# Kernel tuning notes

Measured on AMD Instinct MI355X. Metric: run time of the kernel, lower is better.

Reference implementation:

```python
import jax, jax.numpy as jnp
import numpy as np

DIM = 64
HEADS = 4
N_NODES = 50000
N_EDGES = 800000
NEG_SLOPE = 0.2


def setup_inputs() -> dict:
    key = jax.random.key(0)
    k1, k2, k3, k4, k5 = jax.random.split(key, 5)
    meta_x = jax.random.normal(k1, (N_NODES, DIM), dtype=jnp.float32)
    meta_edge_index = jax.random.randint(k2, (2, N_EDGES), 0, N_NODES, dtype=jnp.int64)
    # GATConv params: shared source/dest Linear (no bias), per-head attention vecs, output bias.
    glorot = float(np.sqrt(2.0 / (DIM + HEADS * DIM)))
    W = jax.random.normal(k3, (DIM, HEADS * DIM), dtype=jnp.float32) * glorot  # x @ W
    att_src = jax.random.normal(k4, (1, HEADS, DIM), dtype=jnp.float32) * glorot
    att_dst = jax.random.normal(k5, (1, HEADS, DIM), dtype=jnp.float32) * glorot
    bias = jnp.zeros((DIM,), dtype=jnp.float32)
    return {"meta_x": meta_x, "meta_edge_index": meta_edge_index,
            "W": W, "att_src": att_src, "att_dst": att_dst, "bias": bias}


def reference(meta_x, meta_edge_index, W, att_src, att_dst, bias):
    N = meta_x.shape[0]
    # PyG GATConv default: add self-loops
    loops = jnp.arange(N, dtype=meta_edge_index.dtype)
    edge = jnp.concatenate([meta_edge_index, jnp.stack([loops, loops])], axis=1)
    src, dst = edge[0], edge[1]

    x = (meta_x @ W).reshape(N, HEADS, DIM)            # [N, H, C]
    a_src = jnp.sum(x * att_src, axis=-1)              # [N, H]
    a_dst = jnp.sum(x * att_dst, axis=-1)              # [N, H]

    logits = a_src[src] + a_dst[dst]                   # [E, H]
    logits = jax.nn.leaky_relu(logits, NEG_SLOPE)

    # segment softmax over edges grouped by destination node
    seg_max = jax.ops.segment_max(logits, dst, num_segments=N)   # [N, H]
    ex = jnp.exp(logits - seg_max[dst])
    seg_sum = jax.ops.segment_sum(ex, dst, num_segments=N)
    alpha = ex / (seg_sum[dst] + 1e-16)                # [E, H]

    msg = x[src] * alpha[:, :, None]                   # [E, H, C]
    out = jax.ops.segment_sum(msg, dst, num_segments=N)  # [N, H, C]
    # concat=False -> mean over heads, then bias
    return out.mean(axis=1) + bias
```

## Files before the change

### kernel.cpp

```cpp
#include <hip/hip_runtime.h>
#include <hip/hip_bf16.h>
#include <math.h>

#define MAXDEG 64

__device__ __forceinline__ float lrelu(float v) { return v > 0.0f ? v : 0.2f * v; }

__global__ void prep_kernel(int4* __restrict__ cnt4, int n4,
                            const float* __restrict__ W, const float* __restrict__ att_src,
                            const float* __restrict__ att_dst, float* __restrict__ wsrc,
                            float* __restrict__ wdst) {
  int idx = blockIdx.x * 256 + threadIdx.x;
  for (int i = idx; i < n4; i += gridDim.x * 256) cnt4[i] = make_int4(0, 0, 0, 0);
  if (blockIdx.x == 0) {
    int t = threadIdx.x;
    int h = t >> 6, k = t & 63;
    const float* wrow = W + (size_t)k * 256 + h * 64;
    const float* as = att_src + h * 64;
    const float* ad = att_dst + h * 64;
    float ss = 0.f, sd = 0.f;
#pragma unroll
    for (int c = 0; c < 64; ++c) {
      float w = wrow[c];
      ss = fmaf(w, as[c], ss);
      sd = fmaf(w, ad[c], sd);
    }
    wsrc[k * 4 + h] = ss;
    wdst[k * 4 + h] = sd;
  }
}

__global__ void nattn_kernel(const float* __restrict__ x, const float4* __restrict__ wsrc4,
                             const float4* __restrict__ wdst4, float4* __restrict__ asrc4,
                             float4* __restrict__ adst4, __hip_bfloat16* __restrict__ xh,
                             int N) {
  int lane = threadIdx.x & 63;
  int n = blockIdx.x * 4 + (threadIdx.x >> 6);
  if (n >= N) return;
  float xv = x[(size_t)n * 64 + lane];
  xh[(size_t)n * 64 + lane] = __float2bfloat16(xv);
  float4 ws = wsrc4[lane], wd = wdst4[lane];
  float s0 = xv * ws.x, s1 = xv * ws.y, s2 = xv * ws.z, s3 = xv * ws.w;
  float d0 = xv * wd.x, d1 = xv * wd.y, d2 = xv * wd.z, d3 = xv * wd.w;
#pragma unroll
  for (int m = 1; m < 64; m <<= 1) {
    s0 += __shfl_xor(s0, m, 64); s1 += __shfl_xor(s1, m, 64);
    s2 += __shfl_xor(s2, m, 64); s3 += __shfl_xor(s3, m, 64);
    d0 += __shfl_xor(d0, m, 64); d1 += __shfl_xor(d1, m, 64);
    d2 += __shfl_xor(d2, m, 64); d3 += __shfl_xor(d3, m, 64);
  }
  if (lane == 0) {
    asrc4[n] = make_float4(s0, s1, s2, s3);
    adst4[n] = make_float4(d0, d1, d2, d3);
  }
}

__global__ void hist_kernel(const int* __restrict__ ei, int* __restrict__ counts,
                            int E, int N) {
  int e = blockIdx.x * 256 + threadIdx.x;
  int ET = E + N;
  if (e >= ET) return;
  int dst = (e < E) ? ei[(size_t)E + e] : (e - E);
  atomicAdd(&counts[dst], 1);
}

__global__ void scatter_kernel(const int* __restrict__ ei, int* __restrict__ cursor,
                               int* __restrict__ src_sorted, int E, int N) {
  int e = blockIdx.x * 256 + threadIdx.x;
  int ET = E + N;
  if (e >= ET) return;
  int src, dst;
  if (e < E) {
    src = ei[e];
    dst = ei[(size_t)E + e];
  } else {
    src = dst = e - E;
  }
  int pos = atomicAdd(&cursor[dst], 1);
  src_sorted[pos] = src;
}

__global__ void hist4_kernel(const int* __restrict__ ei, int* __restrict__ counts,
                             int E, int N) {
  int i = blockIdx.x * 256 + threadIdx.x;
  int E4 = E >> 2;
  if (i < E4) {
    int4 d = ((const int4*)(ei + E))[i];
    atomicAdd(&counts[d.x], 1);
    atomicAdd(&counts[d.y], 1);
    atomicAdd(&counts[d.z], 1);
    atomicAdd(&counts[d.w], 1);
  } else if (i < E4 + N) {
    atomicAdd(&counts[i - E4], 1);
  }
}

__global__ void scatter8_kernel(const int* __restrict__ ei, int* __restrict__ cursor,
                                int* __restrict__ srt, int E, int N) {
  int slice = blockIdx.x & 7;
  int bid = blockIdx.x >> 3;
  int nb = gridDim.x >> 3;
  int chunk = (N + 7) >> 3;
  int lo = slice * chunk;
  int hi = lo + chunk; if (hi > N) hi = N;
  int E4 = E >> 2;
  const int4* s4p = (const int4*)ei;
  const int4* d4p = (const int4*)(ei + E);
  int stride = nb * 256;
  for (int i = bid * 256 + threadIdx.x; i < E4; i += stride) {
    int4 d4 = d4p[i];
    bool bx = (d4.x >= lo && d4.x < hi), by = (d4.y >= lo && d4.y < hi);
    bool bz = (d4.z >= lo && d4.z < hi), bw = (d4.w >= lo && d4.w < hi);
    if (!(bx || by || bz || bw)) continue;
    int4 s4 = s4p[i];
    if (bx) { int p = atomicAdd(&cursor[d4.x], 1); srt[p] = s4.x; }
    if (by) { int p = atomicAdd(&cursor[d4.y], 1); srt[p] = s4.y; }
    if (bz) { int p = atomicAdd(&cursor[d4.z], 1); srt[p] = s4.z; }
    if (bw) { int p = atomicAdd(&cursor[d4.w], 1); srt[p] = s4.w; }
  }
  for (int n = lo + bid * 256 + threadIdx.x; n < hi; n += stride) {
    int p = atomicAdd(&cursor[n], 1);
    srt[p] = n;
  }
}

__global__ void scanA_kernel(const int* __restrict__ cnt, int* __restrict__ tsum, int N) {
  int b = blockIdx.x, t = threadIdx.x;
  int idx = b * 256 + t;
  int v = (idx < N) ? cnt[idx] : 0;
#pragma unroll
  for (int m = 1; m < 64; m <<= 1) v += __shfl_xor(v, m, 64);
  __shared__ int ws[4];
  if ((t & 63) == 0) ws[t >> 6] = v;
  __syncthreads();
  if (t == 0) tsum[b] = ws[0] + ws[1] + ws[2] + ws[3];
}

__global__ void scanBC_kernel(const int* __restrict__ cnt, const int* __restrict__ tsum,
                              int* __restrict__ row, int* __restrict__ cur, int N,
                              int ntiles) {
  __shared__ int tl[256];
  __shared__ int part[256];
  int b = blockIdx.x, t = threadIdx.x;
  int tv = (t < ntiles) ? tsum[t] : 0;
  tl[t] = tv;
  __syncthreads();
  for (int d = 1; d < 256; d <<= 1) {
    int u = (t >= d) ? tl[t - d] : 0;
    __syncthreads();
    tl[t] += u;
    __syncthreads();
  }
  int tileoff = (b == 0) ? 0 : tl[b - 1];
  int idx = b * 256 + t;
  int c = (idx < N) ? cnt[idx] : 0;
  part[t] = c;
  __syncthreads();
  for (int d = 1; d < 256; d <<= 1) {
    int u = (t >= d) ? part[t - d] : 0;
    __syncthreads();
    part[t] += u;
    __syncthreads();
  }
  int exc = part[t] - c + tileoff;
  if (idx < N) {
    row[idx] = exc;
    cur[idx] = exc;
    if (idx == N - 1) row[N] = exc + c;
  }
}

__global__ void scanB_kernel(int* __restrict__ tsum, int ntiles) {
  __shared__ int part[256];
  int t = threadIdx.x;
  int carry = 0;
  for (int b0 = 0; b0 < ntiles; b0 += 256) {
    int idx = b0 + t;
    int v = (idx < ntiles) ? tsum[idx] : 0;
    part[t] = v;
    __syncthreads();
    for (int d = 1; d < 256; d <<= 1) {
      int u = (t >= d) ? part[t - d] : 0;
      __syncthreads();
      part[t] += u;
      __syncthreads();
    }
    if (idx < ntiles) tsum[idx] = part[t] - v + carry;
    carry += part[255];
    __syncthreads();
  }
}

__global__ void scanC_kernel(const int* __restrict__ cnt, const int* __restrict__ tsum,
                             int* __restrict__ row, int* __restrict__ cur, int N) {
  __shared__ int part[256];
  int b = blockIdx.x, t = threadIdx.x;
  int idx = b * 256 + t;
  int c = (idx < N) ? cnt[idx] : 0;
  part[t] = c;
  __syncthreads();
  for (int d = 1; d < 256; d <<= 1) {
    int u = (t >= d) ? part[t - d] : 0;
    __syncthreads();
    part[t] += u;
    __syncthreads();
  }
  int exc = part[t] - c + tsum[b];
  if (idx < N) {
    row[idx] = exc;
    cur[idx] = exc;
    if (idx == N - 1) row[N] = exc + c;
  }
}

__global__ __launch_bounds__(256) void agg_kernel(
    const int* __restrict__ srt, const int* __restrict__ row,
    const float4* __restrict__ asrc4, const float4* __restrict__ adst4,
    const __hip_bfloat16* __restrict__ xh, __hip_bfloat16* __restrict__ agg, int N) {
  __shared__ float4 alL[4][MAXDEG];
  __shared__ int slL[4][MAXDEG];
  int t = threadIdx.x, w = t >> 6, lane = t & 63;
  int n = blockIdx.x * 4 + w;
  if (n >= N) return;
  int start = row[n], end = row[n + 1];
  int deg = end - start;
  float4 ad = adst4[n];
  float t0 = 0.f, t1 = 0.f, t2 = 0.f, t3 = 0.f;
  if (deg <= MAXDEG) {
    for (int b = 0; b < deg; b += 64) {
      if (b + lane < deg) {
        int sl = srt[start + b + lane];
        float4 as = asrc4[sl];
        float4 e;
        e.x = __expf(lrelu(as.x + ad.x));
        e.y = __expf(lrelu(as.y + ad.y));
        e.z = __expf(lrelu(as.z + ad.z));
        e.w = __expf(lrelu(as.w + ad.w));
        alL[w][b + lane] = e;
        slL[w][b + lane] = sl;
        t0 += e.x; t1 += e.y; t2 += e.z; t3 += e.w;
      }
    }
  } else {
    for (int b = start; b < end; b += 64) {
      int idx = b + lane;
      if (idx < end) {
        int sl = srt[idx];
        float4 as = asrc4[sl];
        t0 += __expf(lrelu(as.x + ad.x));
        t1 += __expf(lrelu(as.y + ad.y));
        t2 += __expf(lrelu(as.z + ad.z));
        t3 += __expf(lrelu(as.w + ad.w));
      }
    }
  }
#pragma unroll
  for (int m = 1; m < 64; m <<= 1) {
    t0 += __shfl_xor(t0, m, 64);
    t1 += __shfl_xor(t1, m, 64);
    t2 += __shfl_xor(t2, m, 64);
    t3 += __shfl_xor(t3, m, 64);
  }
  float r0 = 0.25f / (t0 + 1e-16f), r1 = 0.25f / (t1 + 1e-16f);
  float r2 = 0.25f / (t2 + 1e-16f), r3 = 0.25f / (t3 + 1e-16f);
  float a0 = 0.f, a1 = 0.f, a2 = 0.f, a3 = 0.f;
  if (deg <= MAXDEG) {
    int j = 0;
    for (; j + 4 <= deg; j += 4) {
      float4 e0 = alL[w][j], e1 = alL[w][j + 1], e2 = alL[w][j + 2], e3 = alL[w][j + 3];
      int q0 = slL[w][j], q1 = slL[w][j + 1], q2 = slL[w][j + 2], q3 = slL[w][j + 3];
      float v0 = __bfloat162float(xh[(size_t)q0 * 64 + lane]);
      float v1 = __bfloat162float(xh[(size_t)q1 * 64 + lane]);
      float v2 = __bfloat162float(xh[(size_t)q2 * 64 + lane]);
      float v3 = __bfloat162float(xh[(size_t)q3 * 64 + lane]);
      a0 = fmaf(e0.x, v0, a0); a1 = fmaf(e0.y, v0, a1);
      a2 = fmaf(e0.z, v0, a2); a3 = fmaf(e0.w, v0, a3);
      a0 = fmaf(e1.x, v1, a0); a1 = fmaf(e1.y, v1, a1);
      a2 = fmaf(e1.z, v1, a2); a3 = fmaf(e1.w, v1, a3);
      a0 = fmaf(e2.x, v2, a0); a1 = fmaf(e2.y, v2, a1);
      a2 = fmaf(e2.z, v2, a2); a3 = fmaf(e2.w, v2, a3);
      a0 = fmaf(e3.x, v3, a0); a1 = fmaf(e3.y, v3, a1);
      a2 = fmaf(e3.z, v3, a2); a3 = fmaf(e3.w, v3, a3);
    }
    for (; j < deg; ++j) {
      float4 e0 = alL[w][j];
      int q0 = slL[w][j];
      float v0 = __bfloat162float(xh[(size_t)q0 * 64 + lane]);
      a0 = fmaf(e0.x, v0, a0); a1 = fmaf(e0.y, v0, a1);
      a2 = fmaf(e0.z, v0, a2); a3 = fmaf(e0.w, v0, a3);
    }
  } else {
    for (int b = start; b < end; b += 64) {
      int cnt = end - b;
      if (cnt > 64) cnt = 64;
      int idx = b + lane;
      int sl = 0;
      float e0 = 0.f, e1 = 0.f, e2 = 0.f, e3 = 0.f;
      if (idx < end) {
        sl = srt[idx];
        float4 as = asrc4[sl];
        e0 = __expf(lrelu(as.x + ad.x));
        e1 = __expf(lrelu(as.y + ad.y));
        e2 = __expf(lrelu(as.z + ad.z));
        e3 = __expf(lrelu(as.w + ad.w));
      }
      for (int j = 0; j < cnt; ++j) {
        int sj = __shfl(sl, j, 64);
        float b0 = __shfl(e0, j, 64), b1 = __shfl(e1, j, 64);
        float b2 = __shfl(e2, j, 64), b3 = __shfl(e3, j, 64);
        float v = __bfloat162float(xh[(size_t)sj * 64 + lane]);
        a0 = fmaf(b0, v, a0); a1 = fmaf(b1, v, a1);
        a2 = fmaf(b2, v, a2); a3 = fmaf(b3, v, a3);
      }
    }
  }
  __hip_bfloat16* ao = agg + (size_t)n * 256;
  ao[lane] = __float2bfloat16(a0 * r0);
  ao[64 + lane] = __float2bfloat16(a1 * r1);
  ao[128 + lane] = __float2bfloat16(a2 * r2);
  ao[192 + lane] = __float2bfloat16(a3 * r3);
}

__global__ __launch_bounds__(256) void proj_kernel(
    const __hip_bfloat16* __restrict__ agg, const float* __restrict__ W,
    const float* __restrict__ bias, float* __restrict__ out, int N) {
  __shared__ float aggL[4][256];
  __shared__ float pL[4][4][64];
  int t = threadIdx.x, w = t >> 6, lane = t & 63;
  float Wreg[64];
#pragma unroll
  for (int k = 0; k < 64; ++k) Wreg[k] = W[(size_t)k * 256 + w * 64 + lane];
  float bv = bias[lane];
  int ngroups = (N + 3) >> 2;
  for (int g = blockIdx.x; g < ngroups; g += gridDim.x) {
    int n0 = g * 4;
    __syncthreads();
    {
      int nn = n0 + w;
      if (nn < N) {
        ushort4 u = ((const ushort4*)(agg + (size_t)nn * 256))[t & 63];
        float4 f;
        f.x = __bfloat162float(*(__hip_bfloat16*)&u.x);
        f.y = __bfloat162float(*(__hip_bfloat16*)&u.y);
        f.z = __bfloat162float(*(__hip_bfloat16*)&u.z);
        f.w = __bfloat162float(*(__hip_bfloat16*)&u.w);
        *(float4*)&aggL[w][(t & 63) * 4] = f;
      } else {
        *(float4*)&aggL[w][(t & 63) * 4] = make_float4(0.f, 0.f, 0.f, 0.f);
      }
    }
    __syncthreads();
    float acc0 = 0.f, acc1 = 0.f, acc2 = 0.f, acc3 = 0.f;
#pragma unroll
    for (int k4 = 0; k4 < 16; ++k4) {
      float4 av0 = *(const float4*)&aggL[0][w * 64 + k4 * 4];
      float4 av1 = *(const float4*)&aggL[1][w * 64 + k4 * 4];
      float4 av2 = *(const float4*)&aggL[2][w * 64 + k4 * 4];
      float4 av3 = *(const float4*)&aggL[3][w * 64 + k4 * 4];
      float w0 = Wreg[k4 * 4 + 0], w1 = Wreg[k4 * 4 + 1];
      float w2 = Wreg[k4 * 4 + 2], w3 = Wreg[k4 * 4 + 3];
      acc0 = fmaf(av0.x, w0, acc0); acc0 = fmaf(av0.y, w1, acc0);
      acc0 = fmaf(av0.z, w2, acc0); acc0 = fmaf(av0.w, w3, acc0);
      acc1 = fmaf(av1.x, w0, acc1); acc1 = fmaf(av1.y, w1, acc1);
      acc1 = fmaf(av1.z, w2, acc1); acc1 = fmaf(av1.w, w3, acc1);
      acc2 = fmaf(av2.x, w0, acc2); acc2 = fmaf(av2.y, w1, acc2);
      acc2 = fmaf(av2.z, w2, acc2); acc2 = fmaf(av2.w, w3, acc2);
      acc3 = fmaf(av3.x, w0, acc3); acc3 = fmaf(av3.y, w1, acc3);
      acc3 = fmaf(av3.z, w2, acc3); acc3 = fmaf(av3.w, w3, acc3);
    }
    pL[w][0][lane] = acc0;
    pL[w][1][lane] = acc1;
    pL[w][2][lane] = acc2;
    pL[w][3][lane] = acc3;
    __syncthreads();
    int nn = n0 + w;
    if (nn < N) {
      out[(size_t)nn * 64 + lane] = pL[0][w][lane] + pL[1][w][lane] +
                                    pL[2][w][lane] + pL[3][w][lane] + bv;
    }
  }
}

__global__ __launch_bounds__(256) void gatout_kernel(
    const int* __restrict__ srt, const int* __restrict__ row,
    const float4* __restrict__ asrc4, const float4* __restrict__ adst4,
    const float* __restrict__ x, const float* __restrict__ W,
    const float* __restrict__ bias, float* __restrict__ out, int N) {
  __shared__ float4 smem4[320];
  float4 (*alL)[MAXDEG] = (float4(*)[MAXDEG])smem4;
  int (*slL)[MAXDEG] = (int(*)[MAXDEG])(smem4 + 256);
  float (*buf)[4][64] = (float(*)[4][64])smem4;
  int t = threadIdx.x, w = t >> 6, lane = t & 63;
  float Wreg[64];
#pragma unroll
  for (int k = 0; k < 64; ++k) Wreg[k] = W[(size_t)k * 256 + w * 64 + lane];
  float bv = bias[lane];
  int ngroups = (N + 3) >> 2;
  for (int g = blockIdx.x; g < ngroups; g += gridDim.x) {
    int n = g * 4 + w;
    float a0 = 0.f, a1 = 0.f, a2 = 0.f, a3 = 0.f;
    float r0 = 0.f, r1 = 0.f, r2 = 0.f, r3 = 0.f;
    __syncthreads();
    if (n < N) {
      int start = row[n], end = row[n + 1];
      int deg = end - start;
      float4 ad = adst4[n];
      float t0 = 0.f, t1 = 0.f, t2 = 0.f, t3 = 0.f;
      if (deg <= MAXDEG) {
        for (int b = 0; b < deg; b += 64) {
          if (b + lane < deg) {
            int sl = srt[start + b + lane];
            float4 as = asrc4[sl];
            float4 e;
            e.x = __expf(lrelu(as.x + ad.x));
            e.y = __expf(lrelu(as.y + ad.y));
            e.z = __expf(lrelu(as.z + ad.z));
            e.w = __expf(lrelu(as.w + ad.w));
            alL[w][b + lane] = e;
            slL[w][b + lane] = sl;
            t0 += e.x; t1 += e.y; t2 += e.z; t3 += e.w;
          }
        }
      } else {
        for (int b = start; b < end; b += 64) {
          int idx = b + lane;
          if (idx < end) {
            int sl = srt[idx];
            float4 as = asrc4[sl];
            t0 += __expf(lrelu(as.x + ad.x));
            t1 += __expf(lrelu(as.y + ad.y));
            t2 += __expf(lrelu(as.z + ad.z));
            t3 += __expf(lrelu(as.w + ad.w));
          }
        }
      }
#pragma unroll
      for (int m = 1; m < 64; m <<= 1) {
        t0 += __shfl_xor(t0, m, 64);
        t1 += __shfl_xor(t1, m, 64);
        t2 += __shfl_xor(t2, m, 64);
        t3 += __shfl_xor(t3, m, 64);
      }
      r0 = 0.25f / (t0 + 1e-16f); r1 = 0.25f / (t1 + 1e-16f);
      r2 = 0.25f / (t2 + 1e-16f); r3 = 0.25f / (t3 + 1e-16f);
      if (deg <= MAXDEG) {
        int j = 0;
        for (; j + 4 <= deg; j += 4) {
          float4 e0 = alL[w][j], e1 = alL[w][j + 1], e2 = alL[w][j + 2], e3 = alL[w][j + 3];
          int q0 = slL[w][j], q1 = slL[w][j + 1], q2 = slL[w][j + 2], q3 = slL[w][j + 3];
          float v0 = x[(size_t)q0 * 64 + lane];
          float v1 = x[(size_t)q1 * 64 + lane];
          float v2 = x[(size_t)q2 * 64 + lane];
          float v3 = x[(size_t)q3 * 64 + lane];
          a0 = fmaf(e0.x, v0, a0); a1 = fmaf(e0.y, v0, a1);
          a2 = fmaf(e0.z, v0, a2); a3 = fmaf(e0.w, v0, a3);
          a0 = fmaf(e1.x, v1, a0); a1 = fmaf(e1.y, v1, a1);
          a2 = fmaf(e1.z, v1, a2); a3 = fmaf(e1.w, v1, a3);
          a0 = fmaf(e2.x, v2, a0); a1 = fmaf(e2.y, v2, a1);
          a2 = fmaf(e2.z, v2, a2); a3 = fmaf(e2.w, v2, a3);
          a0 = fmaf(e3.x, v3, a0); a1 = fmaf(e3.y, v3, a1);
          a2 = fmaf(e3.z, v3, a2); a3 = fmaf(e3.w, v3, a3);
        }
        for (; j < deg; ++j) {
          float4 e0 = alL[w][j];
          int q0 = slL[w][j];
          float v0 = x[(size_t)q0 * 64 + lane];
          a0 = fmaf(e0.x, v0, a0); a1 = fmaf(e0.y, v0, a1);
          a2 = fmaf(e0.z, v0, a2); a3 = fmaf(e0.w, v0, a3);
        }
      } else {
        for (int b = start; b < end; b += 64) {
          int cnt = end - b;
          if (cnt > 64) cnt = 64;
          int idx = b + lane;
          int sl = 0;
          float e0 = 0.f, e1 = 0.f, e2 = 0.f, e3 = 0.f;
          if (idx < end) {
            sl = srt[idx];
            float4 as = asrc4[sl];
            e0 = __expf(lrelu(as.x + ad.x));
            e1 = __expf(lrelu(as.y + ad.y));
            e2 = __expf(lrelu(as.z + ad.z));
            e3 = __expf(lrelu(as.w + ad.w));
          }
          for (int j = 0; j < cnt; ++j) {
            int sj = __shfl(sl, j, 64);
            float b0 = __shfl(e0, j, 64), b1 = __shfl(e1, j, 64);
            float b2 = __shfl(e2, j, 64), b3 = __shfl(e3, j, 64);
            float v = x[(size_t)sj * 64 + lane];
            a0 = fmaf(b0, v, a0); a1 = fmaf(b1, v, a1);
            a2 = fmaf(b2, v, a2); a3 = fmaf(b3, v, a3);
          }
        }
      }
    }
    __syncthreads();
    buf[w][0][lane] = a0 * r0;
    buf[w][1][lane] = a1 * r1;
    buf[w][2][lane] = a2 * r2;
    buf[w][3][lane] = a3 * r3;
    __syncthreads();
    float acc0 = 0.f, acc1 = 0.f, acc2 = 0.f, acc3 = 0.f;
#pragma unroll
    for (int k4 = 0; k4 < 16; ++k4) {
      float4 av0 = *(const float4*)&buf[0][w][k4 * 4];
      float4 av1 = *(const float4*)&buf[1][w][k4 * 4];
      float4 av2 = *(const float4*)&buf[2][w][k4 * 4];
      float4 av3 = *(const float4*)&buf[3][w][k4 * 4];
      float w0 = Wreg[k4 * 4 + 0], w1 = Wreg[k4 * 4 + 1];
      float w2 = Wreg[k4 * 4 + 2], w3 = Wreg[k4 * 4 + 3];
      acc0 = fmaf(av0.x, w0, acc0); acc0 = fmaf(av0.y, w1, acc0);
      acc0 = fmaf(av0.z, w2, acc0); acc0 = fmaf(av0.w, w3, acc0);
      acc1 = fmaf(av1.x, w0, acc1); acc1 = fmaf(av1.y, w1, acc1);
      acc1 = fmaf(av1.z, w2, acc1); acc1 = fmaf(av1.w, w3, acc1);
      acc2 = fmaf(av2.x, w0, acc2); acc2 = fmaf(av2.y, w1, acc2);
      acc2 = fmaf(av2.z, w2, acc2); acc2 = fmaf(av2.w, w3, acc2);
      acc3 = fmaf(av3.x, w0, acc3); acc3 = fmaf(av3.y, w1, acc3);
      acc3 = fmaf(av3.z, w2, acc3); acc3 = fmaf(av3.w, w3, acc3);
    }
    __syncthreads();
    buf[w][0][lane] = acc0;
    buf[w][1][lane] = acc1;
    buf[w][2][lane] = acc2;
    buf[w][3][lane] = acc3;
    __syncthreads();
    if (n < N) {
      out[(size_t)n * 64 + lane] = buf[0][w][lane] + buf[1][w][lane] +
                                   buf[2][w][lane] + buf[3][w][lane] + bv;
    }
  }
}

extern "C" void kernel_launch(void* const* d_in, const int* in_sizes, int n_in,
                              void* d_out, int out_size, void* d_ws, size_t ws_size,
                              hipStream_t stream) {
  const float* meta_x = (const float*)d_in[0];
  const int* ei = (const int*)d_in[1];
  const float* W = (const float*)d_in[2];
  const float* att_src = (const float*)d_in[3];
  const float* att_dst = (const float*)d_in[4];
  const float* bias = (const float*)d_in[5];
  float* out = (float*)d_out;

  int N = in_sizes[0] / 64;
  int E = in_sizes[1] / 2;
  int ET = E + N;

  char* ws = (char*)d_ws;
  size_t off = 0;
  auto alloc = [&](size_t bytes) {
    size_t o = off;
    off += (bytes + 255) & ~(size_t)255;
    return o;
  };
  size_t o_wsrc = alloc(64 * 4 * sizeof(float));
  size_t o_wdst = alloc(64 * 4 * sizeof(float));
  size_t o_asrc = alloc((size_t)N * 4 * sizeof(float));
  size_t o_adst = alloc((size_t)N * 4 * sizeof(float));
  size_t o_cnt = alloc(((size_t)N + 4) * sizeof(int));
  size_t o_row = alloc(((size_t)N + 1) * sizeof(int));
  size_t o_cur = alloc((size_t)N * sizeof(int));
  size_t o_srt = alloc((size_t)ET * sizeof(int));
  size_t o_ts = alloc((((size_t)N + 255) / 256) * sizeof(int));
  size_t o_xh = alloc((size_t)N * 64 * sizeof(__hip_bfloat16));
  size_t o_agg = alloc((size_t)N * 256 * sizeof(__hip_bfloat16));
  bool split = (ws_size >= off);

  float* wsrc = (float*)(ws + o_wsrc);
  float* wdst = (float*)(ws + o_wdst);
  float4* asrc4 = (float4*)(ws + o_asrc);
  float4* adst4 = (float4*)(ws + o_adst);
  int* cnt = (int*)(ws + o_cnt);
  int* row = (int*)(ws + o_row);
  int* cur = (int*)(ws + o_cur);
  int* srt = (int*)(ws + o_srt);
  int* tsum = (int*)(ws + o_ts);
  __hip_bfloat16* xh = (__hip_bfloat16*)(ws + o_xh);
  __hip_bfloat16* aggp = (__hip_bfloat16*)(ws + o_agg);

  int n4 = (N + 4) >> 2;
  prep_kernel<<<64, 256, 0, stream>>>((int4*)cnt, n4, W, att_src, att_dst, wsrc, wdst);
  nattn_kernel<<<(N + 3) / 4, 256, 0, stream>>>(meta_x, (const float4*)wsrc,
                                                (const float4*)wdst, asrc4, adst4, xh, N);
  if ((E & 3) == 0) {
    int nt4 = (E >> 2) + N;
    hist4_kernel<<<(nt4 + 255) / 256, 256, 0, stream>>>(ei, cnt, E, N);
  } else {
    hist_kernel<<<(ET + 255) / 256, 256, 0, stream>>>(ei, cnt, E, N);
  }
  int ntiles = (N + 255) / 256;
  scanA_kernel<<<ntiles, 256, 0, stream>>>(cnt, tsum, N);
  if (ntiles <= 256) {
    scanBC_kernel<<<ntiles, 256, 0, stream>>>(cnt, tsum, row, cur, N, ntiles);
  } else {
    scanB_kernel<<<1, 256, 0, stream>>>(tsum, ntiles);
    scanC_kernel<<<ntiles, 256, 0, stream>>>(cnt, tsum, row, cur, N);
  }
  if ((E & 3) == 0) {
    scatter8_kernel<<<2048, 256, 0, stream>>>(ei, cur, srt, E, N);
  } else {
    scatter_kernel<<<(ET + 255) / 256, 256, 0, stream>>>(ei, cur, srt, E, N);
  }
  if (split) {
    agg_kernel<<<(N + 3) / 4, 256, 0, stream>>>(srt, row, asrc4, adst4, xh, aggp, N);
    int ngroups = (N + 3) / 4;
    int pgrid = ngroups < 2048 ? ngroups : 2048;
    proj_kernel<<<pgrid, 256, 0, stream>>>(aggp, W, bias, out, N);
  } else {
    int ngroups = (N + 3) / 4;
    int ggrid = ngroups < 2048 ? ngroups : 2048;
    gatout_kernel<<<ggrid, 256, 0, stream>>>(srt, row, asrc4, adst4, meta_x, W, bias, out, N);
  }
}
```

Measured before the change: 186.0 us.

## Fuse histogram with node attention kernel and merge scan passes into one

Merges the destination-degree histogram and the per-node attention/bf16-cast work into one launch, with blocks split by index, so the two independent stages share a grid and one launch is saved. Folds the tile-sum pass into the scan kernel: each block recomputes all tile sums directly from padded counts, removing the scanA launch at the cost of redundant reads. Drops the fused gatout fallback so the split agg/proj path always runs, and halves the proj grid cap. The count buffer is padded to a multiple of 256 so the vectorized tile-sum reads stay in bounds.

Result: no change. 185.6 us (-0.2%).

```diff
diff --git a/kernel.cpp b/kernel.cpp
--- a/kernel.cpp
+++ b/kernel.cpp
@@ -30,6 +30,46 @@
   }
 }
 
+__global__ void nh_kernel(const float* __restrict__ x, const float4* __restrict__ wsrc4,
+                          const float4* __restrict__ wdst4, float4* __restrict__ asrc4,
+                          float4* __restrict__ adst4, __hip_bfloat16* __restrict__ xh,
+                          const int* __restrict__ ei, int* __restrict__ counts,
+                          int E, int N, int nbh) {
+  if (blockIdx.x < nbh) {
+    int i = blockIdx.x * 256 + threadIdx.x;
+    int E4 = E >> 2;
+    if (i < E4) {
+      int4 d = ((const int4*)(ei + E))[i];
+      atomicAdd(&counts[d.x], 1);
+      atomicAdd(&counts[d.y], 1);
+      atomicAdd(&counts[d.z], 1);
+      atomicAdd(&counts[d.w], 1);
+    } else if (i < E4 + N) {
+      atomicAdd(&counts[i - E4], 1);
+    }
+    return;
+  }
+  int lane = threadIdx.x & 63;
+  int n = (blockIdx.x - nbh) * 4 + (threadIdx.x >> 6);
+  if (n >= N) return;
+  float xv = x[(size_t)n * 64 + lane];
+  xh[(size_t)n * 64 + lane] = __float2bfloat16(xv);
+  float4 ws = wsrc4[lane], wd = wdst4[lane];
+  float s0 = xv * ws.x, s1 = xv * ws.y, s2 = xv * ws.z, s3 = xv * ws.w;
+  float d0 = xv * wd.x, d1 = xv * wd.y, d2 = xv * wd.z, d3 = xv * wd.w;
+#pragma unroll
+  for (int m = 1; m < 64; m <<= 1) {
+    s0 += __shfl_xor(s0, m, 64); s1 += __shfl_xor(s1, m, 64);
+    s2 += __shfl_xor(s2, m, 64); s3 += __shfl_xor(s3, m, 64);
+    d0 += __shfl_xor(d0, m, 64); d1 += __shfl_xor(d1, m, 64);
+    d2 += __shfl_xor(d2, m, 64); d3 += __shfl_xor(d3, m, 64);
+  }
+  if (lane == 0) {
+    asrc4[n] = make_float4(s0, s1, s2, s3);
+    adst4[n] = make_float4(d0, d1, d2, d3);
+  }
+}
+
 __global__ void nattn_kernel(const float* __restrict__ x, const float4* __restrict__ wsrc4,
                              const float4* __restrict__ wdst4, float4* __restrict__ asrc4,
                              float4* __restrict__ adst4, __hip_bfloat16* __restrict__ xh,
@@ -78,21 +118,6 @@
   }
   int pos = atomicAdd(&cursor[dst], 1);
   src_sorted[pos] = src;
-}
-
-__global__ void hist4_kernel(const int* __restrict__ ei, int* __restrict__ counts,
-                             int E, int N) {
-  int i = blockIdx.x * 256 + threadIdx.x;
-  int E4 = E >> 2;
-  if (i < E4) {
-    int4 d = ((const int4*)(ei + E))[i];
-    atomicAdd(&counts[d.x], 1);
-    atomicAdd(&counts[d.y], 1);
-    atomicAdd(&counts[d.z], 1);
-    atomicAdd(&counts[d.w], 1);
-  } else if (i < E4 + N) {
-    atomicAdd(&counts[i - E4], 1);
-  }
 }
 
 __global__ void scatter8_kernel(const int* __restrict__ ei, int* __restrict__ cursor,
@@ -124,26 +149,20 @@
   }
 }
 
-__global__ void scanA_kernel(const int* __restrict__ cnt, int* __restrict__ tsum, int N) {
-  int b = blockIdx.x, t = threadIdx.x;
-  int idx = b * 256 + t;
-  int v = (idx < N) ? cnt[idx] : 0;
-#pragma unroll
-  for (int m = 1; m < 64; m <<= 1) v += __shfl_xor(v, m, 64);
-  __shared__ int ws[4];
-  if ((t & 63) == 0) ws[t >> 6] = v;
-  __syncthreads();
-  if (t == 0) tsum[b] = ws[0] + ws[1] + ws[2] + ws[3];
-}
-
-__global__ void scanBC_kernel(const int* __restrict__ cnt, const int* __restrict__ tsum,
-                              int* __restrict__ row, int* __restrict__ cur, int N,
-                              int ntiles) {
+__global__ void scanABC_kernel(const int* __restrict__ cnt, int* __restrict__ row,
+                               int* __restrict__ cur, int N, int ntiles) {
   __shared__ int tl[256];
   __shared__ int part[256];
   int b = blockIdx.x, t = threadIdx.x;
-  int tv = (t < ntiles) ? tsum[t] : 0;
-  tl[t] = tv;
+  int s = 0;
+  if (t < ntiles) {
+    const int4* c4 = (const int4*)cnt + t * 64;
+    for (int i = 0; i < 64; ++i) {
+      int4 v = c4[i];
+      s += v.x + v.y + v.z + v.w;
+    }
+  }
+  tl[t] = s;
   __syncthreads();
   for (int d = 1; d < 256; d <<= 1) {
     int u = (t >= d) ? tl[t - d] : 0;
@@ -168,6 +187,18 @@
     cur[idx] = exc;
     if (idx == N - 1) row[N] = exc + c;
   }
+}
+
+__global__ void scanA_kernel(const int* __restrict__ cnt, int* __restrict__ tsum, int N) {
+  int b = blockIdx.x, t = threadIdx.x;
+  int idx = b * 256 + t;
+  int v = (idx < N) ? cnt[idx] : 0;
+#pragma unroll
+  for (int m = 1; m < 64; m <<= 1) v += __shfl_xor(v, m, 64);
+  __shared__ int ws[4];
+  if ((t & 63) == 0) ws[t >> 6] = v;
+  __syncthreads();
+  if (t == 0) tsum[b] = ws[0] + ws[1] + ws[2] + ws[3];
 }
 
 __global__ void scanB_kernel(int* __restrict__ tsum, int ntiles) {
@@ -381,156 +412,6 @@
   }
 }
 
-__global__ __launch_bounds__(256) void gatout_kernel(
-    const int* __restrict__ srt, const int* __restrict__ row,
-    const float4* __restrict__ asrc4, const float4* __restrict__ adst4,
-    const float* __restrict__ x, const float* __restrict__ W,
-    const float* __restrict__ bias, float* __restrict__ out, int N) {
-  __shared__ float4 smem4[320];
-  float4 (*alL)[MAXDEG] = (float4(*)[MAXDEG])smem4;
-  int (*slL)[MAXDEG] = (int(*)[MAXDEG])(smem4 + 256);
-  float (*buf)[4][64] = (float(*)[4][64])smem4;
-  int t = threadIdx.x, w = t >> 6, lane = t & 63;
-  float Wreg[64];
-#pragma unroll
-  for (int k = 0; k < 64; ++k) Wreg[k] = W[(size_t)k * 256 + w * 64 + lane];
-  float bv = bias[lane];
-  int ngroups = (N + 3) >> 2;
-  for (int g = blockIdx.x; g < ngroups; g += gridDim.x) {
-    int n = g * 4 + w;
-    float a0 = 0.f, a1 = 0.f, a2 = 0.f, a3 = 0.f;
-    float r0 = 0.f, r1 = 0.f, r2 = 0.f, r3 = 0.f;
-    __syncthreads();
-    if (n < N) {
-      int start = row[n], end = row[n + 1];
-      int deg = end - start;
-      float4 ad = adst4[n];
-      float t0 = 0.f, t1 = 0.f, t2 = 0.f, t3 = 0.f;
-      if (deg <= MAXDEG) {
-        for (int b = 0; b < deg; b += 64) {
-          if (b + lane < deg) {
-            int sl = srt[start + b + lane];
-            float4 as = asrc4[sl];
-            float4 e;
-            e.x = __expf(lrelu(as.x + ad.x));
-            e.y = __expf(lrelu(as.y + ad.y));
-            e.z = __expf(lrelu(as.z + ad.z));
-            e.w = __expf(lrelu(as.w + ad.w));
-            alL[w][b + lane] = e;
-            slL[w][b + lane] = sl;
-            t0 += e.x; t1 += e.y; t2 += e.z; t3 += e.w;
-          }
-        }
-      } else {
-        for (int b = start; b < end; b += 64) {
-          int idx = b + lane;
-          if (idx < end) {
-            int sl = srt[idx];
-            float4 as = asrc4[sl];
-            t0 += __expf(lrelu(as.x + ad.x));
-            t1 += __expf(lrelu(as.y + ad.y));
-            t2 += __expf(lrelu(as.z + ad.z));
-            t3 += __expf(lrelu(as.w + ad.w));
-          }
-        }
-      }
-#pragma unroll
-      for (int m = 1; m < 64; m <<= 1) {
-        t0 += __shfl_xor(t0, m, 64);
-        t1 += __shfl_xor(t1, m, 64);
-        t2 += __shfl_xor(t2, m, 64);
-        t3 += __shfl_xor(t3, m, 64);
-      }
-      r0 = 0.25f / (t0 + 1e-16f); r1 = 0.25f / (t1 + 1e-16f);
-      r2 = 0.25f / (t2 + 1e-16f); r3 = 0.25f / (t3 + 1e-16f);
-      if (deg <= MAXDEG) {
-        int j = 0;
-        for (; j + 4 <= deg; j += 4) {
-          float4 e0 = alL[w][j], e1 = alL[w][j + 1], e2 = alL[w][j + 2], e3 = alL[w][j + 3];
-          int q0 = slL[w][j], q1 = slL[w][j + 1], q2 = slL[w][j + 2], q3 = slL[w][j + 3];
-          float v0 = x[(size_t)q0 * 64 + lane];
-          float v1 = x[(size_t)q1 * 64 + lane];
-          float v2 = x[(size_t)q2 * 64 + lane];
-          float v3 = x[(size_t)q3 * 64 + lane];
-          a0 = fmaf(e0.x, v0, a0); a1 = fmaf(e0.y, v0, a1);
-          a2 = fmaf(e0.z, v0, a2); a3 = fmaf(e0.w, v0, a3);
-          a0 = fmaf(e1.x, v1, a0); a1 = fmaf(e1.y, v1, a1);
-          a2 = fmaf(e1.z, v1, a2); a3 = fmaf(e1.w, v1, a3);
-          a0 = fmaf(e2.x, v2, a0); a1 = fmaf(e2.y, v2, a1);
-          a2 = fmaf(e2.z, v2, a2); a3 = fmaf(e2.w, v2, a3);
-          a0 = fmaf(e3.x, v3, a0); a1 = fmaf(e3.y, v3, a1);
-          a2 = fmaf(e3.z, v3, a2); a3 = fmaf(e3.w, v3, a3);
-        }
-        for (; j < deg; ++j) {
-          float4 e0 = alL[w][j];
-          int q0 = slL[w][j];
-          float v0 = x[(size_t)q0 * 64 + lane];
-          a0 = fmaf(e0.x, v0, a0); a1 = fmaf(e0.y, v0, a1);
-          a2 = fmaf(e0.z, v0, a2); a3 = fmaf(e0.w, v0, a3);
-        }
-      } else {
-        for (int b = start; b < end; b += 64) {
-          int cnt = end - b;
-          if (cnt > 64) cnt = 64;
-          int idx = b + lane;
-          int sl = 0;
-          float e0 = 0.f, e1 = 0.f, e2 = 0.f, e3 = 0.f;
-          if (idx < end) {
-            sl = srt[idx];
-            float4 as = asrc4[sl];
-            e0 = __expf(lrelu(as.x + ad.x));
-            e1 = __expf(lrelu(as.y + ad.y));
-            e2 = __expf(lrelu(as.z + ad.z));
-            e3 = __expf(lrelu(as.w + ad.w));
-          }
-          for (int j = 0; j < cnt; ++j) {
-            int sj = __shfl(sl, j, 64);
-            float b0 = __shfl(e0, j, 64), b1 = __shfl(e1, j, 64);
-            float b2 = __shfl(e2, j, 64), b3 = __shfl(e3, j, 64);
-            float v = x[(size_t)sj * 64 + lane];
-            a0 = fmaf(b0, v, a0); a1 = fmaf(b1, v, a1);
-            a2 = fmaf(b2, v, a2); a3 = fmaf(b3, v, a3);
-          }
-        }
-      }
-    }
-    __syncthreads();
-    buf[w][0][lane] = a0 * r0;
-    buf[w][1][lane] = a1 * r1;
-    buf[w][2][lane] = a2 * r2;
-    buf[w][3][lane] = a3 * r3;
-    __syncthreads();
-    float acc0 = 0.f, acc1 = 0.f, acc2 = 0.f, acc3 = 0.f;
-#pragma unroll
-    for (int k4 = 0; k4 < 16; ++k4) {
-      float4 av0 = *(const float4*)&buf[0][w][k4 * 4];
-      float4 av1 = *(const float4*)&buf[1][w][k4 * 4];
-      float4 av2 = *(const float4*)&buf[2][w][k4 * 4];
-      float4 av3 = *(const float4*)&buf[3][w][k4 * 4];
-      float w0 = Wreg[k4 * 4 + 0], w1 = Wreg[k4 * 4 + 1];
-      float w2 = Wreg[k4 * 4 + 2], w3 = Wreg[k4 * 4 + 3];
-      acc0 = fmaf(av0.x, w0, acc0); acc0 = fmaf(av0.y, w1, acc0);
-      acc0 = fmaf(av0.z, w2, acc0); acc0 = fmaf(av0.w, w3, acc0);
-      acc1 = fmaf(av1.x, w0, acc1); acc1 = fmaf(av1.y, w1, acc1);
-      acc1 = fmaf(av1.z, w2, acc1); acc1 = fmaf(av1.w, w3, acc1);
-      acc2 = fmaf(av2.x, w0, acc2); acc2 = fmaf(av2.y, w1, acc2);
-      acc2 = fmaf(av2.z, w2, acc2); acc2 = fmaf(av2.w, w3, acc2);
-      acc3 = fmaf(av3.x, w0, acc3); acc3 = fmaf(av3.y, w1, acc3);
-      acc3 = fmaf(av3.z, w2, acc3); acc3 = fmaf(av3.w, w3, acc3);
-    }
-    __syncthreads();
-    buf[w][0][lane] = acc0;
-    buf[w][1][lane] = acc1;
-    buf[w][2][lane] = acc2;
-    buf[w][3][lane] = acc3;
-    __syncthreads();
-    if (n < N) {
-      out[(size_t)n * 64 + lane] = buf[0][w][lane] + buf[1][w][lane] +
-                                   buf[2][w][lane] + buf[3][w][lane] + bv;
-    }
-  }
-}
-
 extern "C" void kernel_launch(void* const* d_in, const int* in_sizes, int n_in,
                               void* d_out, int out_size, void* d_ws, size_t ws_size,
                               hipStream_t stream) {
@@ -545,6 +426,7 @@
   int N = in_sizes[0] / 64;
   int E = in_sizes[1] / 2;
   int ET = E + N;
+  int ntiles = (N + 255) / 256;
 
   char* ws = (char*)d_ws;
   size_t off = 0;
@@ -557,14 +439,15 @@
   size_t o_wdst = alloc(64 * 4 * sizeof(float));
   size_t o_asrc = alloc((size_t)N * 4 * sizeof(float));
   size_t o_adst = alloc((size_t)N * 4 * sizeof(float));
-  size_t o_cnt = alloc(((size_t)N + 4) * sizeof(int));
+  size_t o_cnt = alloc((size_t)ntiles * 256 * sizeof(int));
   size_t o_row = alloc(((size_t)N + 1) * sizeof(int));
   size_t o_cur = alloc((size_t)N * sizeof(int));
   size_t o_srt = alloc((size_t)ET * sizeof(int));
-  size_t o_ts = alloc((((size_t)N + 255) / 256) * sizeof(int));
+  size_t o_ts = alloc((size_t)ntiles * sizeof(int));
   size_t o_xh = alloc((size_t)N * 64 * sizeof(__hip_bfloat16));
   size_t o_agg = alloc((size_t)N * 256 * sizeof(__hip_bfloat16));
   bool split = (ws_size >= off);
+  (void)split;
 
   float* wsrc = (float*)(ws + o_wsrc);
   float* wdst = (float*)(ws + o_wdst);
@@ -578,37 +461,37 @@
   __hip_bfloat16* xh = (__hip_bfloat16*)(ws + o_xh);
   __hip_bfloat16* aggp = (__hip_bfloat16*)(ws + o_agg);
 
-  int n4 = (N + 4) >> 2;
+  int n4 = ntiles * 64;
   prep_kernel<<<64, 256, 0, stream>>>((int4*)cnt, n4, W, att_src, att_dst, wsrc, wdst);
-  nattn_kernel<<<(N + 3) / 4, 256, 0, stream>>>(meta_x, (const float4*)wsrc,
-                                                (const float4*)wdst, asrc4, adst4, xh, N);
+
   if ((E & 3) == 0) {
-    int nt4 = (E >> 2) + N;
-    hist4_kernel<<<(nt4 + 255) / 256, 256, 0, stream>>>(ei, cnt, E, N);
-  } else {
+    int nbh = ((E >> 2) + N + 255) / 256;
+    int nbn = (N + 3) / 4;
+    nh_kernel<<<nbh + nbn, 256, 0, stream>>>(meta_x, (const float4*)wsrc,
+                                             (const float4*)wdst, asrc4, adst4, xh,
+                                             ei, cnt, E, N, nbh);
+  } else {
+    nattn_kernel<<<(N + 3) / 4, 256, 0, stream>>>(meta_x, (const float4*)wsrc,
+                                                  (const float4*)wdst, asrc4, adst4, xh, N);
     hist_kernel<<<(ET + 255) / 256, 256, 0, stream>>>(ei, cnt, E, N);
   }
-  int ntiles = (N + 255) / 256;
-  scanA_kernel<<<ntiles, 256, 0, stream>>>(cnt, tsum, N);
+
   if (ntiles <= 256) {
-    scanBC_kernel<<<ntiles, 256, 0, stream>>>(cnt, tsum, row, cur, N, ntiles);
-  } else {
+    scanABC_kernel<<<ntiles, 256, 0, stream>>>(cnt, row, cur, N, ntiles);
+  } else {
+    scanA_kernel<<<ntiles, 256, 0, stream>>>(cnt, tsum, N);
     scanB_kernel<<<1, 256, 0, stream>>>(tsum, ntiles);
     scanC_kernel<<<ntiles, 256, 0, stream>>>(cnt, tsum, row, cur, N);
   }
+
   if ((E & 3) == 0) {
     scatter8_kernel<<<2048, 256, 0, stream>>>(ei, cur, srt, E, N);
   } else {
     scatter_kernel<<<(ET + 255) / 256, 256, 0, stream>>>(ei, cur, srt, E, N);
   }
-  if (split) {
-    agg_kernel<<<(N + 3) / 4, 256, 0, stream>>>(srt, row, asrc4, adst4, xh, aggp, N);
-    int ngroups = (N + 3) / 4;
-    int pgrid = ngroups < 2048 ? ngroups : 2048;
-    proj_kernel<<<pgrid, 256, 0, stream>>>(aggp, W, bias, out, N);
-  } else {
-    int ngroups = (N + 3) / 4;
-    int ggrid = ngroups < 2048 ? ngroups : 2048;
-    gatout_kernel<<<ggrid, 256, 0, stream>>>(srt, row, asrc4, adst4, meta_x, W, bias, out, N);
-  }
-}
+
+  agg_kernel<<<(N + 3) / 4, 256, 0, stream>>>(srt, row, asrc4, adst4, xh, aggp, N);
+  int ngroups = (N + 3) / 4;
+  int pgrid = ngroups < 1024 ? ngroups : 1024;
+  proj_kernel<<<pgrid, 256, 0, stream>>>(aggp, W, bias, out, N);
+}
```
